# Performance work log

Hardware: AMD Instinct MI355X
Metric: run time of the kernel (lower is better)

## Reference

```python
import jax, jax.numpy as jnp
import numpy as np

N_LAYERS = 2
D_MODEL = 1024
D_INNER = 2 * D_MODEL
D_STATE = 16
D_CONV = 4
DT_RANK = D_MODEL // 16  # 64
B_SZ, L = 1, 2048
EPS = 1e-5


def layernorm(x, w, b):
    mu = jnp.mean(x, axis=-1, keepdims=True)
    var = jnp.mean(jnp.square(x - mu), axis=-1, keepdims=True)
    return (x - mu) * jax.lax.rsqrt(var + EPS) * w + b


def mamba(x, in_w, cw, cb, xp_w, dtp_w, dtp_b, A_log, Dp, out_w):
    # x: [B, L, D_MODEL]
    Bn, Ln, _ = x.shape
    xz = jnp.einsum('bld,ed->ble', x, in_w)          # [B,L,2*D_INNER]
    xc, z = jnp.split(xz, 2, axis=-1)
    # causal depthwise conv1d (kernel D_CONV)
    xp = jnp.pad(xc, ((0, 0), (D_CONV - 1, 0), (0, 0)))
    xc = sum(xp[:, k:k + Ln, :] * cw[:, k] for k in range(D_CONV)) + cb
    xc = jax.nn.silu(xc)
    dbl = jnp.einsum('ble,re->blr', xc, xp_w)        # [B,L,DT_RANK+2*D_STATE]
    dt, Bm, Cm = jnp.split(dbl, [DT_RANK, DT_RANK + D_STATE], axis=-1)
    dt = jax.nn.softplus(jnp.einsum('blr,er->ble', dt, dtp_w) + dtp_b)  # [B,L,E]
    A = -jnp.exp(A_log)                              # [E,N], strictly negative
    dA = jnp.exp(dt[..., None] * A)                  # [B,L,E,N]
    dBu = (dt * xc)[..., None] * Bm[:, :, None, :]   # [B,L,E,N]

    def step(h, inp):
        dA_t, dBu_t, C_t = inp
        h = dA_t * h + dBu_t                         # [B,E,N]
        y = jnp.einsum('ben,bn->be', h, C_t)
        return h, y

    h0 = jnp.zeros((Bn, D_INNER, D_STATE), dA.dtype)
    _, ys = jax.lax.scan(step, h0, (dA.transpose(1, 0, 2, 3),
                                    dBu.transpose(1, 0, 2, 3),
                                    Cm.transpose(1, 0, 2)))
    y = ys.transpose(1, 0, 2) + xc * Dp              # [B,L,E]
    y = y * jax.nn.silu(z)
    return jnp.einsum('ble,de->bld', y, out_w)       # [B,L,D_MODEL]


def setup_inputs() -> dict:
    key = jax.random.key(0)
    ks = jax.random.split(key, 12)
    s = 0.02
    dt_init = np.log(np.expm1(0.01)).astype(np.float32)  # softplus^-1(0.01)
    A_row = jnp.log(jnp.arange(1, D_STATE + 1, dtype=jnp.float32))
    return {
        'x': jax.random.normal(ks[0], (B_SZ, L, D_MODEL), jnp.float32),
        'ln_w': jnp.ones((N_LAYERS, D_MODEL), jnp.float32),
        'ln_b': jnp.zeros((N_LAYERS, D_MODEL), jnp.float32),
        'in_proj_w': jax.random.normal(ks[1], (N_LAYERS, 2 * D_INNER, D_MODEL)) * s,
        'conv_w': jax.random.normal(ks[2], (N_LAYERS, D_INNER, D_CONV)) * 0.2,
        'conv_b': jnp.zeros((N_LAYERS, D_INNER), jnp.float32),
        'x_proj_w': jax.random.normal(ks[3], (N_LAYERS, DT_RANK + 2 * D_STATE, D_INNER)) * s,
        'dt_proj_w': jax.random.normal(ks[4], (N_LAYERS, D_INNER, DT_RANK)) * (DT_RANK ** -0.5),
        'dt_proj_b': jnp.full((N_LAYERS, D_INNER), dt_init),
        'A_log': jnp.broadcast_to(A_row, (N_LAYERS, D_INNER, D_STATE)).copy(),
        'D_skip': jnp.ones((N_LAYERS, D_INNER), jnp.float32),
        'out_proj_w': jax.random.normal(ks[5], (N_LAYERS, D_MODEL, D_INNER)) * s,
        'norm_f_w': jnp.ones((D_MODEL,), jnp.float32),
        'norm_f_b': jnp.zeros((D_MODEL,), jnp.float32),
    }


def reference(x, ln_w, ln_b, in_proj_w, conv_w, conv_b, x_proj_w, dt_proj_w,
              dt_proj_b, A_log, D_skip, out_proj_w, norm_f_w, norm_f_b):
    for i in range(N_LAYERS):
        h = layernorm(x, ln_w[i], ln_b[i])
        h = mamba(h, in_proj_w[i], conv_w[i], conv_b[i], x_proj_w[i],
                  dt_proj_w[i], dt_proj_b[i], A_log[i], D_skip[i], out_proj_w[i])
        x = h + x  # residual (dropout/drop_path are identity in eval)
    return layernorm(x, norm_f_w, norm_f_b)
```

## Files before the change

kernel.cpp:

```cpp
#include <hip/hip_runtime.h>
#include <hip/hip_bf16.h>
#include <math.h>

#define LSEQ 2048
#define DMODEL 1024
#define DINNER 2048
#define DSTATE 16
#define DCONV 4
#define DTRANK 64
#define RPROJ 96

#define CHUNK 16
#define NCHUNK (LSEQ / CHUNK)

#define XSPLIT 4

typedef __attribute__((ext_vector_type(8))) short bf16x8;
typedef __attribute__((ext_vector_type(4))) float f32x4;

__device__ __forceinline__ float softplusf(float x) {
    return (x > 20.f) ? x : log1pf(__expf(x));
}
__device__ __forceinline__ float siluf(float x) {
    return x / (1.f + __expf(-x));
}
__device__ __forceinline__ short f2bf(float f) {
    union { float f; unsigned u; } v; v.f = f;
    unsigned r = v.u + 0x7FFFu + ((v.u >> 16) & 1u);
    return (short)(r >> 16);
}
__device__ __forceinline__ float bf2f(short h) {
    union { unsigned u; float f; } v;
    v.u = ((unsigned)(unsigned short)h) << 16;
    return v.f;
}

__device__ __forceinline__ void cvt8(const float* __restrict__ s,
                                     short* __restrict__ d, int i) {
    const float4 a = *(const float4*)(s + i);
    const float4 b = *(const float4*)(s + i + 4);
    alignas(16) short h[8];
    h[0] = f2bf(a.x); h[1] = f2bf(a.y); h[2] = f2bf(a.z); h[3] = f2bf(a.w);
    h[4] = f2bf(b.x); h[5] = f2bf(b.y); h[6] = f2bf(b.z); h[7] = f2bf(b.w);
    *(uint4*)(d + i) = *(const uint4*)h;
}

__global__ __launch_bounds__(256) void cvt_weights(
    const float* __restrict__ s0, short* __restrict__ d0, int n0,
    const float* __restrict__ s1, short* __restrict__ d1, int n1,
    const float* __restrict__ s2, short* __restrict__ d2, int n2,
    const float* __restrict__ s3, short* __restrict__ d3, int n3)
{
    int i = (blockIdx.x * 256 + threadIdx.x) * 8;
    if (i < n0) { cvt8(s0, d0, i); return; }
    i -= n0;
    if (i < n1) { cvt8(s1, d1, i); return; }
    i -= n1;
    if (i < n2) { cvt8(s2, d2, i); return; }
    i -= n2;
    if (i < n3) { cvt8(s3, d3, i); return; }
}

__global__ __launch_bounds__(256) void ln_kernel(
    const float* __restrict__ x, const float* __restrict__ w,
    const float* __restrict__ b, float* __restrict__ outf,
    short* __restrict__ outb)
{
    __shared__ float s1[256], s2[256];
    const int row = blockIdx.x;
    const int tid = threadIdx.x;
    const float* xr = x + (size_t)row * DMODEL;
    float v[4];
    float s = 0.f, sq = 0.f;
#pragma unroll
    for (int k = 0; k < 4; k++) {
        v[k] = xr[k * 256 + tid];
        s += v[k];
        sq += v[k] * v[k];
    }
    s1[tid] = s; s2[tid] = sq;
    __syncthreads();
    for (int off = 128; off > 0; off >>= 1) {
        if (tid < off) { s1[tid] += s1[tid + off]; s2[tid] += s2[tid + off]; }
        __syncthreads();
    }
    const float mu = s1[0] * (1.f / DMODEL);
    const float var = s2[0] * (1.f / DMODEL) - mu * mu;
    const float rstd = rsqrtf(var + 1e-5f);
#pragma unroll
    for (int k = 0; k < 4; k++) {
        const int i = k * 256 + tid;
        const float o = (v[k] - mu) * rstd * w[i] + b[i];
        if (outf) outf[(size_t)row * DMODEL + i] = o;
        if (outb) outb[(size_t)row * DMODEL + i] = f2bf(o);
    }
}

template<int MI, int NJ, int MODE>
__global__ __launch_bounds__(256) void gemm_mfma(
    const short* __restrict__ A, int lda,
    const short* __restrict__ W, int ldw,
    float* __restrict__ Cf, short* __restrict__ Cb, int ldc,
    int M, int N, int K,
    const float* __restrict__ resid)
{
    constexpr int BM = 32 * MI;
    constexpr int BN = 32 * NJ;
    constexpr int AISS = BM / 32;
    constexpr int WISS = BN / 32;
    __shared__ alignas(16) short As[BM * 64];
    __shared__ alignas(16) short Ws[BN * 64];

    const int tid = threadIdx.x;
    const int lane = tid & 63;
    const int w = tid >> 6;
    const int wr = w >> 1, wc = w & 1;
    const int row0 = blockIdx.y * BM;
    const int col0 = blockIdx.x * BN;
    const int kbeg = blockIdx.z * K;

    const int srow = tid >> 3;
    const int dch  = tid & 7;
    const int skch = (dch ^ (srow & 7)) * 8;

    f32x4 acc[MI][NJ];
#pragma unroll
    for (int i = 0; i < MI; i++)
#pragma unroll
        for (int j = 0; j < NJ; j++) acc[i][j] = (f32x4)0.f;

    const int lrow = lane & 15;
    const int q = lane >> 4;

    for (int kt = kbeg; kt < kbeg + K; kt += 64) {
        __syncthreads();
#pragma unroll
        for (int j = 0; j < AISS; j++) {
            const short* gp = A + (size_t)(row0 + j * 32 + srow) * lda + kt + skch;
            __builtin_amdgcn_global_load_lds(
                (const __attribute__((address_space(1))) void*)gp,
                (__attribute__((address_space(3))) void*)(&As[j * 2048 + tid * 8]),
                16, 0, 0);
        }
#pragma unroll
        for (int j = 0; j < WISS; j++) {
            const int wrow = col0 + j * 32 + srow;
            if (wrow < N) {
                const short* gp = W + (size_t)wrow * ldw + kt + skch;
                __builtin_amdgcn_global_load_lds(
                    (const __attribute__((address_space(1))) void*)gp,
                    (__attribute__((address_space(3))) void*)(&Ws[j * 2048 + tid * 8]),
                    16, 0, 0);
            }
        }
        __syncthreads();

#pragma unroll
        for (int ks = 0; ks < 2; ks++) {
            bf16x8 af[MI], bfr[NJ];
#pragma unroll
            for (int i = 0; i < MI; i++) {
                const int R = wr * (16 * MI) + i * 16 + lrow;
                const int pc = (ks * 4 + q) ^ (R & 7);
                af[i] = *(const bf16x8*)&As[R * 64 + pc * 8];
            }
#pragma unroll
            for (int j = 0; j < NJ; j++) {
                const int R = wc * (16 * NJ) + j * 16 + lrow;
                const int pc = (ks * 4 + q) ^ (R & 7);
                bfr[j] = *(const bf16x8*)&Ws[R * 64 + pc * 8];
            }
#pragma unroll
            for (int i = 0; i < MI; i++)
#pragma unroll
                for (int j = 0; j < NJ; j++)
                    acc[i][j] = __builtin_amdgcn_mfma_f32_16x16x32_bf16(
                        af[i], bfr[j], acc[i][j], 0, 0, 0);
        }
    }

    const int rbase = row0 + wr * (16 * MI);
    const int cbase = col0 + wc * (16 * NJ);
#pragma unroll
    for (int i = 0; i < MI; i++) {
#pragma unroll
        for (int j = 0; j < NJ; j++) {
            const int gcol = cbase + j * 16 + lrow;
            if (gcol < N) {
#pragma unroll
                for (int r = 0; r < 4; r++) {
                    const int grow = rbase + i * 16 + (lane >> 4) * 4 + r;
                    float v = acc[i][j][r];
                    if (MODE == 2) {
                        Cf[(size_t)grow * ldc + gcol] =
                            v + resid[(size_t)grow * ldc + gcol];
                    } else if (MODE == 3) {
                        Cb[(size_t)grow * ldc + gcol] = f2bf(v);
                    } else {
                        atomicAdd(&Cf[(size_t)grow * ldc + gcol], v);
                    }
                }
            }
        }
    }
}

__global__ __launch_bounds__(256) void dtproj_kernel(
    const float* __restrict__ dbl,
    const short* __restrict__ dtp_w,
    const float* __restrict__ dtp_b,
    short* __restrict__ dt_bf)
{
    __shared__ alignas(16) short As[64 * 32];
    __shared__ alignas(16) short Ws[128 * 32];
    const int tid = threadIdx.x;
    const int lane = tid & 63;
    const int w = tid >> 6;
    const int wr = w >> 1, wc = w & 1;
    const int row0 = blockIdx.y * 64;
    const int col0 = blockIdx.x * 128;
    const int srow = tid >> 2;
    const int skch = ((tid & 3) ^ ((srow >> 1) & 3)) * 8;
    const int lrow = lane & 15;
    const int q = lane >> 4;

    f32x4 acc[2][4];
#pragma unroll
    for (int i = 0; i < 2; i++)
#pragma unroll
        for (int j = 0; j < 4; j++) acc[i][j] = (f32x4)0.f;

#pragma unroll
    for (int kt = 0; kt < 64; kt += 32) {
        __syncthreads();
        {
            const float* gp = dbl + (size_t)(row0 + srow) * RPROJ + kt + skch;
            const float4 a = *(const float4*)gp;
            const float4 b = *(const float4*)(gp + 4);
            alignas(16) short h[8];
            h[0] = f2bf(a.x); h[1] = f2bf(a.y); h[2] = f2bf(a.z); h[3] = f2bf(a.w);
            h[4] = f2bf(b.x); h[5] = f2bf(b.y); h[6] = f2bf(b.z); h[7] = f2bf(b.w);
            *(uint4*)(As + tid * 8) = *(const uint4*)h;
        }
#pragma unroll
        for (int j = 0; j < 2; j++) {
            const short* gp = dtp_w + (size_t)(col0 + j * 64 + srow) * DTRANK + kt + skch;
            __builtin_amdgcn_global_load_lds(
                (const __attribute__((address_space(1))) void*)gp,
                (__attribute__((address_space(3))) void*)(&Ws[j * 2048 + tid * 8]),
                16, 0, 0);
        }
        __syncthreads();

        bf16x8 af[2], bfr[4];
#pragma unroll
        for (int i = 0; i < 2; i++) {
            const int R = wr * 32 + i * 16 + lrow;
            af[i] = *(const bf16x8*)&As[R * 32 + ((q ^ ((R >> 1) & 3)) * 8)];
        }
#pragma unroll
        for (int j = 0; j < 4; j++) {
            const int R = wc * 64 + j * 16 + lrow;
            bfr[j] = *(const bf16x8*)&Ws[R * 32 + ((q ^ ((R >> 1) & 3)) * 8)];
        }
#pragma unroll
        for (int i = 0; i < 2; i++)
#pragma unroll
            for (int j = 0; j < 4; j++)
                acc[i][j] = __builtin_amdgcn_mfma_f32_16x16x32_bf16(
                    af[i], bfr[j], acc[i][j], 0, 0, 0);
    }

    const int rbase = row0 + wr * 32;
    const int cbase = col0 + wc * 64;
#pragma unroll
    for (int i = 0; i < 2; i++)
#pragma unroll
        for (int j = 0; j < 4; j++) {
            const int gcol = cbase + j * 16 + lrow;
#pragma unroll
            for (int r = 0; r < 4; r++) {
                const int grow = rbase + i * 16 + (lane >> 4) * 4 + r;
                dt_bf[(size_t)grow * DINNER + gcol] =
                    f2bf(softplusf(acc[i][j][r] + dtp_b[gcol]));
            }
        }
}

__global__ __launch_bounds__(256) void conv_silu_kernel(
    const short* __restrict__ xzb, const float* __restrict__ cw,
    const float* __restrict__ cb, short* __restrict__ xcb,
    float* __restrict__ dbl_zero)
{
    const int g = blockIdx.x * 256 + threadIdx.x;
    if (g < (LSEQ * RPROJ) / 4)
        *(float4*)(dbl_zero + g * 4) = make_float4(0.f, 0.f, 0.f, 0.f);
    const int t = g >> 8;
    const int c0 = (g & 255) * 8;
    float acc[8];
#pragma unroll
    for (int j = 0; j < 8; j++) acc[j] = cb[c0 + j];
#pragma unroll
    for (int k = 0; k < DCONV; k++) {
        const int tt = t - (DCONV - 1) + k;
        if (tt >= 0) {
            const bf16x8 v = *(const bf16x8*)(xzb + (size_t)tt * (2 * DINNER) + c0);
#pragma unroll
            for (int j = 0; j < 8; j++)
                acc[j] += bf2f(v[j]) * cw[(c0 + j) * DCONV + k];
        }
    }
    alignas(16) short h[8];
#pragma unroll
    for (int j = 0; j < 8; j++) h[j] = f2bf(siluf(acc[j]));
    *(uint4*)(xcb + (size_t)t * DINNER + c0) = *(const uint4*)h;
}

__global__ __launch_bounds__(256) void scan_pass1(
    const short* __restrict__ dtb,
    const short* __restrict__ xcb,
    const float* __restrict__ dbl,
    const float* __restrict__ A_log,
    float* __restrict__ S,
    float* __restrict__ sumdt)
{
    const int e = blockIdx.x * 256 + threadIdx.x;
    const int c = blockIdx.y;
    float a[DSTATE];
#pragma unroll
    for (int n = 0; n < DSTATE; n++) a[n] = -__expf(A_log[(size_t)e * DSTATE + n]);
    float h[DSTATE];
#pragma unroll
    for (int n = 0; n < DSTATE; n++) h[n] = 0.f;
    float sd = 0.f;

    __shared__ float sBC[CHUNK][32];
    for (int i = threadIdx.x; i < CHUNK * 32; i += 256) {
        const int tl = i >> 5, j = i & 31;
        sBC[tl][j] = dbl[(size_t)(c * CHUNK + tl) * RPROJ + DTRANK + j];
    }
    __syncthreads();

    const size_t rb = (size_t)c * CHUNK * DINNER + e;
    short dt_c = dtb[rb], xc_c = xcb[rb];
#pragma unroll
    for (int tl = 0; tl < CHUNK; tl++) {
        short dt_n = 0, xc_n = 0;
        if (tl + 1 < CHUNK) {
            dt_n = dtb[rb + (size_t)(tl + 1) * DINNER];
            xc_n = xcb[rb + (size_t)(tl + 1) * DINNER];
        }
        const float dtv = bf2f(dt_c);
        const float du = dtv * bf2f(xc_c);
        sd += dtv;
#pragma unroll
        for (int n = 0; n < DSTATE; n++) {
            const float dA = __expf(dtv * a[n]);
            h[n] = dA * h[n] + du * sBC[tl][n];
        }
        dt_c = dt_n; xc_c = xc_n;
    }
    sumdt[(size_t)c * DINNER + e] = sd;
#pragma unroll
    for (int n = 0; n < DSTATE; n++)
        S[((size_t)c * DSTATE + n) * DINNER + e] = h[n];
}

__global__ __launch_bounds__(256) void scan_pass2(
    const float* __restrict__ A_log,
    const float* __restrict__ sumdt,
    float* __restrict__ S)
{
    const int idx = blockIdx.x * 256 + threadIdx.x;
    const int e = idx & (DINNER - 1);
    const int n = idx >> 11;
    const float a = -__expf(A_log[(size_t)e * DSTATE + n]);
    const size_t base = (size_t)n * DINNER + e;
    const size_t cstr = (size_t)DSTATE * DINNER;
    float H = 0.f;
    for (int c = 0; c < NCHUNK; c += 4) {
        const float sc0 = S[base + (size_t)(c + 0) * cstr];
        const float sc1 = S[base + (size_t)(c + 1) * cstr];
        const float sc2 = S[base + (size_t)(c + 2) * cstr];
        const float sc3 = S[base + (size_t)(c + 3) * cstr];
        const float sd0 = sumdt[(size_t)(c + 0) * DINNER + e];
        const float sd1 = sumdt[(size_t)(c + 1) * DINNER + e];
        const float sd2 = sumdt[(size_t)(c + 2) * DINNER + e];
        const float sd3 = sumdt[(size_t)(c + 3) * DINNER + e];
        S[base + (size_t)(c + 0) * cstr] = H;
        H = __expf(a * sd0) * H + sc0;
        S[base + (size_t)(c + 1) * cstr] = H;
        H = __expf(a * sd1) * H + sc1;
        S[base + (size_t)(c + 2) * cstr] = H;
        H = __expf(a * sd2) * H + sc2;
        S[base + (size_t)(c + 3) * cstr] = H;
        H = __expf(a * sd3) * H + sc3;
    }
}

__global__ __launch_bounds__(256) void scan_pass3(
    const short* __restrict__ dtb,
    const short* __restrict__ xcb,
    const float* __restrict__ dbl,
    const short* __restrict__ xzb,
    const float* __restrict__ A_log,
    const float* __restrict__ Dp,
    const float* __restrict__ S,
    short* __restrict__ yb)
{
    const int e = blockIdx.x * 256 + threadIdx.x;
    const int c = blockIdx.y;
    float a[DSTATE];
#pragma unroll
    for (int n = 0; n < DSTATE; n++) a[n] = -__expf(A_log[(size_t)e * DSTATE + n]);
    float h[DSTATE];
#pragma unroll
    for (int n = 0; n < DSTATE; n++)
        h[n] = S[((size_t)c * DSTATE + n) * DINNER + e];
    const float dskip = Dp[e];

    __shared__ float sBC[CHUNK][32];
    for (int i = threadIdx.x; i < CHUNK * 32; i += 256) {
        const int tl = i >> 5, j = i & 31;
        sBC[tl][j] = dbl[(size_t)(c * CHUNK + tl) * RPROJ + DTRANK + j];
    }
    __syncthreads();

    const size_t rb = (size_t)c * CHUNK * DINNER + e;
    const size_t zb = (size_t)c * CHUNK * (2 * DINNER) + DINNER + e;
    short dt_c = dtb[rb], xc_c = xcb[rb], z_c = xzb[zb];
#pragma unroll
    for (int tl = 0; tl < CHUNK; tl++) {
        short dt_n = 0, xc_n = 0, z_n = 0;
        if (tl + 1 < CHUNK) {
            dt_n = dtb[rb + (size_t)(tl + 1) * DINNER];
            xc_n = xcb[rb + (size_t)(tl + 1) * DINNER];
            z_n = xzb[zb + (size_t)(tl + 1) * (2 * DINNER)];
        }
        const float dtv = bf2f(dt_c);
        const float xcv = bf2f(xc_c);
        const float du = dtv * xcv;
        float yv = 0.f;
#pragma unroll
        for (int n = 0; n < DSTATE; n++) {
            const float dA = __expf(dtv * a[n]);
            h[n] = dA * h[n] + du * sBC[tl][n];
            yv += h[n] * sBC[tl][16 + n];
        }
        yv = (yv + xcv * dskip) * siluf(bf2f(z_c));
        yb[rb + (size_t)tl * DINNER] = f2bf(yv);
        dt_c = dt_n; xc_c = xc_n; z_c = z_n;
    }
}

extern "C" void kernel_launch(void* const* d_in, const int* in_sizes, int n_in,
                              void* d_out, int out_size, void* d_ws, size_t ws_size,
                              hipStream_t stream) {
    const float* x_in   = (const float*)d_in[0];
    const float* ln_w   = (const float*)d_in[1];
    const float* ln_b   = (const float*)d_in[2];
    const float* in_w   = (const float*)d_in[3];
    const float* conv_w = (const float*)d_in[4];
    const float* conv_b = (const float*)d_in[5];
    const float* xp_w   = (const float*)d_in[6];
    const float* dtp_w  = (const float*)d_in[7];
    const float* dtp_b  = (const float*)d_in[8];
    const float* A_log  = (const float*)d_in[9];
    const float* D_skip = (const float*)d_in[10];
    const float* out_w  = (const float*)d_in[11];
    const float* nf_w   = (const float*)d_in[12];
    const float* nf_b   = (const float*)d_in[13];
    float* out = (float*)d_out;

    float* w = (float*)d_ws;
    float* buf_x = w; w += (size_t)LSEQ * DMODEL;
    float* dbl   = w; w += (size_t)LSEQ * RPROJ;
    float* Sbuf  = w; w += (size_t)NCHUNK * DSTATE * DINNER;
    float* sumdt = w; w += (size_t)NCHUNK * DINNER;
    short* h_bf    = (short*)w; w += (size_t)LSEQ * DMODEL / 2;
    short* xz_bf   = (short*)w; w += (size_t)LSEQ * 2 * DINNER / 2;
    short* xc_bf   = (short*)w; w += (size_t)LSEQ * DINNER / 2;
    short* dt_bf   = (short*)w; w += (size_t)LSEQ * DINNER / 2;
    short* y_bf    = (short*)w; w += (size_t)LSEQ * DINNER / 2;
    short* in_w_bf  = (short*)w; w += (size_t)2 * (2 * DINNER) * DMODEL / 2;
    short* xp_w_bf  = (short*)w; w += (size_t)2 * RPROJ * DINNER / 2;
    short* dtp_w_bf = (short*)w; w += (size_t)2 * DINNER * DTRANK / 2;
    short* out_w_bf = (short*)w; w += (size_t)2 * DMODEL * DINNER / 2;

    {
        const int n1 = 2 * (2 * DINNER) * DMODEL;
        const int n2 = 2 * RPROJ * DINNER;
        const int n3 = 2 * DMODEL * DINNER;
        const int n4 = 2 * DINNER * DTRANK;
        const int total = n1 + n2 + n3 + n4;
        cvt_weights<<<dim3(total / (256 * 8)), dim3(256), 0, stream>>>(
            in_w, in_w_bf, n1, xp_w, xp_w_bf, n2,
            out_w, out_w_bf, n3, dtp_w, dtp_w_bf, n4);
    }

    for (int layer = 0; layer < 2; layer++) {
        const float* resid_src = (layer == 0) ? x_in : buf_x;
        ln_kernel<<<dim3(LSEQ), dim3(256), 0, stream>>>(
            resid_src, ln_w + layer * DMODEL, ln_b + layer * DMODEL,
            nullptr, h_bf);
        gemm_mfma<4, 4, 3><<<dim3((2 * DINNER) / 128, LSEQ / 128), dim3(256), 0, stream>>>(
            h_bf, DMODEL, in_w_bf + (size_t)layer * 2 * DINNER * DMODEL, DMODEL,
            nullptr, xz_bf, 2 * DINNER, LSEQ, 2 * DINNER, DMODEL, nullptr);
        conv_silu_kernel<<<dim3((LSEQ * DINNER / 8) / 256), dim3(256), 0, stream>>>(
            xz_bf, conv_w + (size_t)layer * DINNER * DCONV, conv_b + layer * DINNER,
            xc_bf, dbl);
        gemm_mfma<2, 2, 6><<<dim3(2, LSEQ / 64, XSPLIT), dim3(256), 0, stream>>>(
            xc_bf, DINNER, xp_w_bf + (size_t)layer * RPROJ * DINNER, DINNER,
            dbl, nullptr, RPROJ, LSEQ, RPROJ, DINNER / XSPLIT, nullptr);
        dtproj_kernel<<<dim3(DINNER / 128, LSEQ / 64), dim3(256), 0, stream>>>(
            dbl, dtp_w_bf + (size_t)layer * DINNER * DTRANK,
            dtp_b + layer * DINNER, dt_bf);
        const float* Al = A_log + (size_t)layer * DINNER * DSTATE;
        scan_pass1<<<dim3(DINNER / 256, NCHUNK), dim3(256), 0, stream>>>(
            dt_bf, xc_bf, dbl, Al, Sbuf, sumdt);
        scan_pass2<<<dim3((DINNER * DSTATE) / 256), dim3(256), 0, stream>>>(
            Al, sumdt, Sbuf);
        scan_pass3<<<dim3(DINNER / 256, NCHUNK), dim3(256), 0, stream>>>(
            dt_bf, xc_bf, dbl, xz_bf, Al, D_skip + layer * DINNER, Sbuf, y_bf);
        gemm_mfma<4, 2, 2><<<dim3(DMODEL / 64, LSEQ / 128), dim3(256), 0, stream>>>(
            y_bf, DINNER, out_w_bf + (size_t)layer * DMODEL * DINNER, DINNER,
            buf_x, nullptr, DMODEL, LSEQ, DMODEL, DINNER, resid_src);
    }
    ln_kernel<<<dim3(LSEQ), dim3(256), 0, stream>>>(buf_x, nf_w, nf_b, out, nullptr);
}
```

Baseline: 456.9 us.

## Fuse whole Mamba forward into one cooperative persistent kernel with grid syncs

Replaces the sequence of roughly twenty kernel launches with a single cooperative kernel of 512 blocks that runs every phase (weight conversion, layernorm, the GEMMs, conv, dt projection, the three scan passes) separated by grid.sync. LayerNorm now does one row per wavefront with shuffle reductions instead of a shared-memory tree. The out-projection GEMM tile shrinks to 64x64 and block-to-tile mappings are swizzled to fit the fixed grid. It aims to remove launch overhead and tail gaps between kernels, at the cost of grid-wide barriers, a fixed block count that may leave some phases underparallelised, and 2-blocks-per-CU occupancy limits. A fallback multi-kernel path is kept in case the cooperative launch is not possible.

After: 481.7 us. +5.4%, slower.

```diff
diff --git a/kernel.cpp b/kernel.cpp
--- a/kernel.cpp
+++ b/kernel.cpp
@@ -1,6 +1,9 @@
 #include <hip/hip_runtime.h>
+#include <hip/hip_cooperative_groups.h>
 #include <hip/hip_bf16.h>
 #include <math.h>
+
+namespace cg = cooperative_groups;
 
 #define LSEQ 2048
 #define DMODEL 1024
@@ -14,6 +17,7 @@
 #define NCHUNK (LSEQ / CHUNK)
 
 #define XSPLIT 4
+#define NBLK 512
 
 typedef __attribute__((ext_vector_type(8))) short bf16x8;
 typedef __attribute__((ext_vector_type(4))) float f32x4;
@@ -45,80 +49,82 @@
     *(uint4*)(d + i) = *(const uint4*)h;
 }
 
-__global__ __launch_bounds__(256) void cvt_weights(
-    const float* __restrict__ s0, short* __restrict__ d0, int n0,
-    const float* __restrict__ s1, short* __restrict__ d1, int n1,
-    const float* __restrict__ s2, short* __restrict__ d2, int n2,
-    const float* __restrict__ s3, short* __restrict__ d3, int n3)
-{
-    int i = (blockIdx.x * 256 + threadIdx.x) * 8;
-    if (i < n0) { cvt8(s0, d0, i); return; }
-    i -= n0;
-    if (i < n1) { cvt8(s1, d1, i); return; }
-    i -= n1;
-    if (i < n2) { cvt8(s2, d2, i); return; }
-    i -= n2;
-    if (i < n3) { cvt8(s3, d3, i); return; }
-}
-
-__global__ __launch_bounds__(256) void ln_kernel(
+__device__ __forceinline__ void cvt_phase(
+    const float* __restrict__ in_w, short* __restrict__ in_w_bf,
+    const float* __restrict__ xp_w, short* __restrict__ xp_w_bf,
+    const float* __restrict__ out_w, short* __restrict__ out_w_bf,
+    const float* __restrict__ dtp_w, short* __restrict__ dtp_w_bf,
+    int g0, int gstride)
+{
+    const int n1 = 2 * (2 * DINNER) * DMODEL;
+    const int n2 = 2 * RPROJ * DINNER;
+    const int n3 = 2 * DMODEL * DINNER;
+    const int n4 = 2 * DINNER * DTRANK;
+    const int total8 = (n1 + n2 + n3 + n4) / 8;
+    for (int g = g0; g < total8; g += gstride) {
+        int i = g * 8;
+        if (i < n1) { cvt8(in_w, in_w_bf, i); continue; }
+        i -= n1;
+        if (i < n2) { cvt8(xp_w, xp_w_bf, i); continue; }
+        i -= n2;
+        if (i < n3) { cvt8(out_w, out_w_bf, i); continue; }
+        i -= n3;
+        cvt8(dtp_w, dtp_w_bf, i);
+    }
+}
+
+__device__ __forceinline__ void ln_phase(
     const float* __restrict__ x, const float* __restrict__ w,
     const float* __restrict__ b, float* __restrict__ outf,
-    short* __restrict__ outb)
-{
-    __shared__ float s1[256], s2[256];
-    const int row = blockIdx.x;
-    const int tid = threadIdx.x;
+    short* __restrict__ outb, int bid, int tid)
+{
+    const int wv = tid >> 6, lane = tid & 63;
+    const int row = bid * 4 + wv;
     const float* xr = x + (size_t)row * DMODEL;
-    float v[4];
+    float v[16];
     float s = 0.f, sq = 0.f;
 #pragma unroll
-    for (int k = 0; k < 4; k++) {
-        v[k] = xr[k * 256 + tid];
+    for (int k = 0; k < 16; k++) {
+        v[k] = xr[k * 64 + lane];
         s += v[k];
         sq += v[k] * v[k];
     }
-    s1[tid] = s; s2[tid] = sq;
-    __syncthreads();
-    for (int off = 128; off > 0; off >>= 1) {
-        if (tid < off) { s1[tid] += s1[tid + off]; s2[tid] += s2[tid + off]; }
-        __syncthreads();
-    }
-    const float mu = s1[0] * (1.f / DMODEL);
-    const float var = s2[0] * (1.f / DMODEL) - mu * mu;
+#pragma unroll
+    for (int off = 32; off > 0; off >>= 1) {
+        s += __shfl_xor(s, off, 64);
+        sq += __shfl_xor(sq, off, 64);
+    }
+    const float mu = s * (1.f / DMODEL);
+    const float var = sq * (1.f / DMODEL) - mu * mu;
     const float rstd = rsqrtf(var + 1e-5f);
 #pragma unroll
-    for (int k = 0; k < 4; k++) {
-        const int i = k * 256 + tid;
+    for (int k = 0; k < 16; k++) {
+        const int i = k * 64 + lane;
         const float o = (v[k] - mu) * rstd * w[i] + b[i];
         if (outf) outf[(size_t)row * DMODEL + i] = o;
-        if (outb) outb[(size_t)row * DMODEL + i] = f2bf(o);
+        else      outb[(size_t)row * DMODEL + i] = f2bf(o);
     }
 }
 
 template<int MI, int NJ, int MODE>
-__global__ __launch_bounds__(256) void gemm_mfma(
+__device__ __forceinline__ void gemm_phase(
+    unsigned char* smemraw,
     const short* __restrict__ A, int lda,
     const short* __restrict__ W, int ldw,
     float* __restrict__ Cf, short* __restrict__ Cb, int ldc,
-    int M, int N, int K,
-    const float* __restrict__ resid)
+    int N, int K, int row0, int col0, int kbeg,
+    const float* __restrict__ resid, int tid)
 {
     constexpr int BM = 32 * MI;
     constexpr int BN = 32 * NJ;
     constexpr int AISS = BM / 32;
     constexpr int WISS = BN / 32;
-    __shared__ alignas(16) short As[BM * 64];
-    __shared__ alignas(16) short Ws[BN * 64];
-
-    const int tid = threadIdx.x;
+    short* As = (short*)smemraw;
+    short* Ws = (short*)(smemraw + (size_t)BM * 64 * 2);
+
     const int lane = tid & 63;
     const int w = tid >> 6;
     const int wr = w >> 1, wc = w & 1;
-    const int row0 = blockIdx.y * BM;
-    const int col0 = blockIdx.x * BN;
-    const int kbeg = blockIdx.z * K;
-
     const int srow = tid >> 3;
     const int dch  = tid & 7;
     const int skch = (dch ^ (srow & 7)) * 8;
@@ -205,20 +211,19 @@
     }
 }
 
-__global__ __launch_bounds__(256) void dtproj_kernel(
+__device__ __forceinline__ void dtproj_phase(
+    unsigned char* smemraw,
     const float* __restrict__ dbl,
     const short* __restrict__ dtp_w,
     const float* __restrict__ dtp_b,
-    short* __restrict__ dt_bf)
-{
-    __shared__ alignas(16) short As[64 * 32];
-    __shared__ alignas(16) short Ws[128 * 32];
-    const int tid = threadIdx.x;
+    short* __restrict__ dt_bf,
+    int row0, int col0, int tid)
+{
+    short* As = (short*)smemraw;
+    short* Ws = (short*)(smemraw + 64 * 32 * 2);
     const int lane = tid & 63;
     const int w = tid >> 6;
     const int wr = w >> 1, wc = w & 1;
-    const int row0 = blockIdx.y * 64;
-    const int col0 = blockIdx.x * 128;
     const int srow = tid >> 2;
     const int skch = ((tid & 3) ^ ((srow >> 1) & 3)) * 8;
     const int lrow = lane & 15;
@@ -287,45 +292,43 @@
         }
 }
 
-__global__ __launch_bounds__(256) void conv_silu_kernel(
+__device__ __forceinline__ void conv_phase(
     const short* __restrict__ xzb, const float* __restrict__ cw,
     const float* __restrict__ cb, short* __restrict__ xcb,
-    float* __restrict__ dbl_zero)
-{
-    const int g = blockIdx.x * 256 + threadIdx.x;
-    if (g < (LSEQ * RPROJ) / 4)
-        *(float4*)(dbl_zero + g * 4) = make_float4(0.f, 0.f, 0.f, 0.f);
-    const int t = g >> 8;
-    const int c0 = (g & 255) * 8;
-    float acc[8];
-#pragma unroll
-    for (int j = 0; j < 8; j++) acc[j] = cb[c0 + j];
-#pragma unroll
-    for (int k = 0; k < DCONV; k++) {
-        const int tt = t - (DCONV - 1) + k;
-        if (tt >= 0) {
-            const bf16x8 v = *(const bf16x8*)(xzb + (size_t)tt * (2 * DINNER) + c0);
-#pragma unroll
-            for (int j = 0; j < 8; j++)
-                acc[j] += bf2f(v[j]) * cw[(c0 + j) * DCONV + k];
-        }
-    }
-    alignas(16) short h[8];
-#pragma unroll
-    for (int j = 0; j < 8; j++) h[j] = f2bf(siluf(acc[j]));
-    *(uint4*)(xcb + (size_t)t * DINNER + c0) = *(const uint4*)h;
-}
-
-__global__ __launch_bounds__(256) void scan_pass1(
-    const short* __restrict__ dtb,
-    const short* __restrict__ xcb,
-    const float* __restrict__ dbl,
-    const float* __restrict__ A_log,
-    float* __restrict__ S,
-    float* __restrict__ sumdt)
-{
-    const int e = blockIdx.x * 256 + threadIdx.x;
-    const int c = blockIdx.y;
+    float* __restrict__ dbl_zero, int gid0, int gstride)
+{
+    for (int g = gid0; g < (LSEQ * DINNER) / 8; g += gstride) {
+        if (g < (LSEQ * RPROJ) / 4)
+            *(float4*)(dbl_zero + g * 4) = make_float4(0.f, 0.f, 0.f, 0.f);
+        const int t = g >> 8;
+        const int c0 = (g & 255) * 8;
+        float acc[8];
+#pragma unroll
+        for (int j = 0; j < 8; j++) acc[j] = cb[c0 + j];
+#pragma unroll
+        for (int k = 0; k < DCONV; k++) {
+            const int tt = t - (DCONV - 1) + k;
+            if (tt >= 0) {
+                const bf16x8 v = *(const bf16x8*)(xzb + (size_t)tt * (2 * DINNER) + c0);
+#pragma unroll
+                for (int j = 0; j < 8; j++)
+                    acc[j] += bf2f(v[j]) * cw[(c0 + j) * DCONV + k];
+            }
+        }
+        alignas(16) short h[8];
+#pragma unroll
+        for (int j = 0; j < 8; j++) h[j] = f2bf(siluf(acc[j]));
+        *(uint4*)(xcb + (size_t)t * DINNER + c0) = *(const uint4*)h;
+    }
+}
+
+__device__ __forceinline__ void scan1_job(
+    int eb, int c, int tid, float* sBC,
+    const short* __restrict__ dtb, const short* __restrict__ xcb,
+    const float* __restrict__ dbl, const float* __restrict__ A_log,
+    float* __restrict__ S, float* __restrict__ sumdt)
+{
+    const int e = eb * 256 + tid;
     float a[DSTATE];
 #pragma unroll
     for (int n = 0; n < DSTATE; n++) a[n] = -__expf(A_log[(size_t)e * DSTATE + n]);
@@ -334,10 +337,10 @@
     for (int n = 0; n < DSTATE; n++) h[n] = 0.f;
     float sd = 0.f;
 
-    __shared__ float sBC[CHUNK][32];
-    for (int i = threadIdx.x; i < CHUNK * 32; i += 256) {
+    __syncthreads();
+    for (int i = tid; i < CHUNK * 32; i += 256) {
         const int tl = i >> 5, j = i & 31;
-        sBC[tl][j] = dbl[(size_t)(c * CHUNK + tl) * RPROJ + DTRANK + j];
+        sBC[tl * 32 + j] = dbl[(size_t)(c * CHUNK + tl) * RPROJ + DTRANK + j];
     }
     __syncthreads();
 
@@ -356,7 +359,7 @@
 #pragma unroll
         for (int n = 0; n < DSTATE; n++) {
             const float dA = __expf(dtv * a[n]);
-            h[n] = dA * h[n] + du * sBC[tl][n];
+            h[n] = dA * h[n] + du * sBC[tl * 32 + n];
         }
         dt_c = dt_n; xc_c = xc_n;
     }
@@ -366,12 +369,10 @@
         S[((size_t)c * DSTATE + n) * DINNER + e] = h[n];
 }
 
-__global__ __launch_bounds__(256) void scan_pass2(
-    const float* __restrict__ A_log,
-    const float* __restrict__ sumdt,
-    float* __restrict__ S)
-{
-    const int idx = blockIdx.x * 256 + threadIdx.x;
+__device__ __forceinline__ void scan2_phase(
+    const float* __restrict__ A_log, const float* __restrict__ sumdt,
+    float* __restrict__ S, int idx)
+{
     const int e = idx & (DINNER - 1);
     const int n = idx >> 11;
     const float a = -__expf(A_log[(size_t)e * DSTATE + n]);
@@ -398,18 +399,14 @@
     }
 }
 
-__global__ __launch_bounds__(256) void scan_pass3(
-    const short* __restrict__ dtb,
-    const short* __restrict__ xcb,
-    const float* __restrict__ dbl,
-    const short* __restrict__ xzb,
-    const float* __restrict__ A_log,
-    const float* __restrict__ Dp,
-    const float* __restrict__ S,
-    short* __restrict__ yb)
-{
-    const int e = blockIdx.x * 256 + threadIdx.x;
-    const int c = blockIdx.y;
+__device__ __forceinline__ void scan3_job(
+    int eb, int c, int tid, float* sBC,
+    const short* __restrict__ dtb, const short* __restrict__ xcb,
+    const float* __restrict__ dbl, const short* __restrict__ xzb,
+    const float* __restrict__ A_log, const float* __restrict__ Dp,
+    const float* __restrict__ S, short* __restrict__ yb)
+{
+    const int e = eb * 256 + tid;
     float a[DSTATE];
 #pragma unroll
     for (int n = 0; n < DSTATE; n++) a[n] = -__expf(A_log[(size_t)e * DSTATE + n]);
@@ -419,10 +416,10 @@
         h[n] = S[((size_t)c * DSTATE + n) * DINNER + e];
     const float dskip = Dp[e];
 
-    __shared__ float sBC[CHUNK][32];
-    for (int i = threadIdx.x; i < CHUNK * 32; i += 256) {
+    __syncthreads();
+    for (int i = tid; i < CHUNK * 32; i += 256) {
         const int tl = i >> 5, j = i & 31;
-        sBC[tl][j] = dbl[(size_t)(c * CHUNK + tl) * RPROJ + DTRANK + j];
+        sBC[tl * 32 + j] = dbl[(size_t)(c * CHUNK + tl) * RPROJ + DTRANK + j];
     }
     __syncthreads();
 
@@ -444,8 +441,8 @@
 #pragma unroll
         for (int n = 0; n < DSTATE; n++) {
             const float dA = __expf(dtv * a[n]);
-            h[n] = dA * h[n] + du * sBC[tl][n];
-            yv += h[n] * sBC[tl][16 + n];
+            h[n] = dA * h[n] + du * sBC[tl * 32 + n];
+            yv += h[n] * sBC[tl * 32 + 16 + n];
         }
         yv = (yv + xcv * dskip) * siluf(bf2f(z_c));
         yb[rb + (size_t)tl * DINNER] = f2bf(yv);
@@ -453,25 +450,173 @@
     }
 }
 
+struct MegaParams {
+    const float *x_in, *ln_w, *ln_b, *in_w, *conv_w, *conv_b, *xp_w, *dtp_w,
+                *dtp_b, *A_log, *D_skip, *out_w, *nf_w, *nf_b;
+    float* out;
+    float *buf_x, *dbl, *Sbuf, *sumdt;
+    short *h_bf, *xz_bf, *xc_bf, *dt_bf, *y_bf;
+    short *in_w_bf, *xp_w_bf, *dtp_w_bf, *out_w_bf;
+};
+
+__global__ __launch_bounds__(256, 2) void mega_kernel(MegaParams p)
+{
+    cg::grid_group grid = cg::this_grid();
+    __shared__ alignas(16) unsigned char smem[32768];
+    const int bid = blockIdx.x;
+    const int tid = threadIdx.x;
+
+    cvt_phase(p.in_w, p.in_w_bf, p.xp_w, p.xp_w_bf, p.out_w, p.out_w_bf,
+              p.dtp_w, p.dtp_w_bf, bid * 256 + tid, NBLK * 256);
+    grid.sync();
+
+    for (int layer = 0; layer < 2; layer++) {
+        const float* resid = layer ? p.buf_x : p.x_in;
+        ln_phase(resid, p.ln_w + layer * DMODEL, p.ln_b + layer * DMODEL,
+                 nullptr, p.h_bf, bid, tid);
+        grid.sync();
+        {
+            const int swz = (bid & 7) * 64 + (bid >> 3);
+            const int tx = swz & 31, ty = swz >> 5;
+            gemm_phase<4, 4, 3>(smem,
+                p.h_bf, DMODEL,
+                p.in_w_bf + (size_t)layer * 2 * DINNER * DMODEL, DMODEL,
+                nullptr, p.xz_bf, 2 * DINNER,
+                2 * DINNER, DMODEL, ty * 128, tx * 128, 0, nullptr, tid);
+        }
+        grid.sync();
+        conv_phase(p.xz_bf, p.conv_w + (size_t)layer * DINNER * DCONV,
+                   p.conv_b + layer * DINNER, p.xc_bf, p.dbl,
+                   bid * 256 + tid, NBLK * 256);
+        grid.sync();
+        if (bid < 2 * 32 * XSPLIT) {
+            const int jx = bid & 1, jy = (bid >> 1) & 31, jz = bid >> 6;
+            gemm_phase<2, 2, 6>(smem,
+                p.xc_bf, DINNER,
+                p.xp_w_bf + (size_t)layer * RPROJ * DINNER, DINNER,
+                p.dbl, nullptr, RPROJ,
+                RPROJ, DINNER / XSPLIT, jy * 64, jx * 64,
+                jz * (DINNER / XSPLIT), nullptr, tid);
+        }
+        grid.sync();
+        {
+            const int jx = bid & 15, jy = bid >> 4;
+            dtproj_phase(smem, p.dbl,
+                         p.dtp_w_bf + (size_t)layer * DINNER * DTRANK,
+                         p.dtp_b + layer * DINNER, p.dt_bf,
+                         jy * 64, jx * 128, tid);
+        }
+        grid.sync();
+        {
+            const float* Al = p.A_log + (size_t)layer * DINNER * DSTATE;
+            float* sBC = (float*)smem;
+#pragma unroll
+            for (int jj = 0; jj < 2; jj++) {
+                const int job = bid * 2 + jj;
+                scan1_job(job & 7, job >> 3, tid, sBC,
+                          p.dt_bf, p.xc_bf, p.dbl, Al, p.Sbuf, p.sumdt);
+            }
+        }
+        grid.sync();
+        if (bid < (DINNER * DSTATE) / 256) {
+            const float* Al = p.A_log + (size_t)layer * DINNER * DSTATE;
+            scan2_phase(Al, p.sumdt, p.Sbuf, bid * 256 + tid);
+        }
+        grid.sync();
+        {
+            const float* Al = p.A_log + (size_t)layer * DINNER * DSTATE;
+            float* sBC = (float*)smem;
+#pragma unroll
+            for (int jj = 0; jj < 2; jj++) {
+                const int job = bid * 2 + jj;
+                scan3_job(job & 7, job >> 3, tid, sBC,
+                          p.dt_bf, p.xc_bf, p.dbl, p.xz_bf, Al,
+                          p.D_skip + layer * DINNER, p.Sbuf, p.y_bf);
+            }
+        }
+        grid.sync();
+        {
+            const int swz = (bid & 7) * 64 + (bid >> 3);
+            const int jx = swz & 15, jy = swz >> 4;
+            gemm_phase<2, 2, 2>(smem,
+                p.y_bf, DINNER,
+                p.out_w_bf + (size_t)layer * DMODEL * DINNER, DINNER,
+                p.buf_x, nullptr, DMODEL,
+                DMODEL, DINNER, jy * 64, jx * 64, 0, resid, tid);
+        }
+        grid.sync();
+    }
+    ln_phase(p.buf_x, p.nf_w, p.nf_b, p.out, nullptr, bid, tid);
+}
+
+__global__ __launch_bounds__(256) void cvt_g(
+    const float* in_w, short* in_w_bf, const float* xp_w, short* xp_w_bf,
+    const float* out_w, short* out_w_bf, const float* dtp_w, short* dtp_w_bf)
+{
+    cvt_phase(in_w, in_w_bf, xp_w, xp_w_bf, out_w, out_w_bf, dtp_w, dtp_w_bf,
+              blockIdx.x * 256 + threadIdx.x, gridDim.x * 256);
+}
+
+__global__ __launch_bounds__(256) void ln_g(
+    const float* x, const float* w, const float* b, float* outf, short* outb)
+{
+    ln_phase(x, w, b, outf, outb, blockIdx.x, threadIdx.x);
+}
+
+template<int MI, int NJ, int MODE>
+__global__ __launch_bounds__(256) void gemm_g(
+    const short* A, int lda, const short* W, int ldw,
+    float* Cf, short* Cb, int ldc, int N, int K, const float* resid)
+{
+    __shared__ alignas(16) unsigned char smem[(32 * MI + 32 * NJ) * 64 * 2];
+    gemm_phase<MI, NJ, MODE>(smem, A, lda, W, ldw, Cf, Cb, ldc, N, K,
+                             blockIdx.y * 32 * MI, blockIdx.x * 32 * NJ,
+                             blockIdx.z * K, resid, threadIdx.x);
+}
+
+__global__ __launch_bounds__(256) void conv_g(
+    const short* xzb, const float* cw, const float* cb, short* xcb,
+    float* dbl_zero)
+{
+    conv_phase(xzb, cw, cb, xcb, dbl_zero,
+               blockIdx.x * 256 + threadIdx.x, gridDim.x * 256);
+}
+
+__global__ __launch_bounds__(256) void dtproj_g(
+    const float* dbl, const short* dtp_w, const float* dtp_b, short* dt_bf)
+{
+    __shared__ alignas(16) unsigned char smem[(64 + 128) * 32 * 2];
+    dtproj_phase(smem, dbl, dtp_w, dtp_b, dt_bf,
+                 blockIdx.y * 64, blockIdx.x * 128, threadIdx.x);
+}
+
+__global__ __launch_bounds__(256) void scan1_g(
+    const short* dtb, const short* xcb, const float* dbl,
+    const float* A_log, float* S, float* sumdt)
+{
+    __shared__ float sBC[CHUNK * 32];
+    scan1_job(blockIdx.x, blockIdx.y, threadIdx.x, sBC,
+              dtb, xcb, dbl, A_log, S, sumdt);
+}
+
+__global__ __launch_bounds__(256) void scan2_g(
+    const float* A_log, const float* sumdt, float* S)
+{
+    scan2_phase(A_log, sumdt, S, blockIdx.x * 256 + threadIdx.x);
+}
+
+__global__ __launch_bounds__(256) void scan3_g(
+    const short* dtb, const short* xcb, const float* dbl, const short* xzb,
+    const float* A_log, const float* Dp, const float* S, short* yb)
+{
+    __shared__ float sBC[CHUNK * 32];
+    scan3_job(blockIdx.x, blockIdx.y, threadIdx.x, sBC,
+              dtb, xcb, dbl, xzb, A_log, Dp, S, yb);
+}
+
 extern "C" void kernel_launch(void* const* d_in, const int* in_sizes, int n_in,
                               void* d_out, int out_size, void* d_ws, size_t ws_size,
                               hipStream_t stream) {
-    const float* x_in   = (const float*)d_in[0];
-    const float* ln_w   = (const float*)d_in[1];
-    const float* ln_b   = (const float*)d_in[2];
-    const float* in_w   = (const float*)d_in[3];
-    const float* conv_w = (const float*)d_in[4];
-    const float* conv_b = (const float*)d_in[5];
-    const float* xp_w   = (const float*)d_in[6];
-    const float* dtp_w  = (const float*)d_in[7];
-    const float* dtp_b  = (const float*)d_in[8];
-    const float* A_log  = (const float*)d_in[9];
-    const float* D_skip = (const float*)d_in[10];
-    const float* out_w  = (const float*)d_in[11];
-    const float* nf_w   = (const float*)d_in[12];
-    const float* nf_b   = (const float*)d_in[13];
-    float* out = (float*)d_out;
-
     float* w = (float*)d_ws;
     float* buf_x = w; w += (size_t)LSEQ * DMODEL;
     float* dbl   = w; w += (size_t)LSEQ * RPROJ;
@@ -487,44 +632,82 @@
     short* dtp_w_bf = (short*)w; w += (size_t)2 * DINNER * DTRANK / 2;
     short* out_w_bf = (short*)w; w += (size_t)2 * DMODEL * DINNER / 2;
 
-    {
-        const int n1 = 2 * (2 * DINNER) * DMODEL;
-        const int n2 = 2 * RPROJ * DINNER;
-        const int n3 = 2 * DMODEL * DINNER;
-        const int n4 = 2 * DINNER * DTRANK;
-        const int total = n1 + n2 + n3 + n4;
-        cvt_weights<<<dim3(total / (256 * 8)), dim3(256), 0, stream>>>(
-            in_w, in_w_bf, n1, xp_w, xp_w_bf, n2,
-            out_w, out_w_bf, n3, dtp_w, dtp_w_bf, n4);
-    }
-
+    MegaParams p;
+    p.x_in   = (const float*)d_in[0];
+    p.ln_w   = (const float*)d_in[1];
+    p.ln_b   = (const float*)d_in[2];
+    p.in_w   = (const float*)d_in[3];
+    p.conv_w = (const float*)d_in[4];
+    p.conv_b = (const float*)d_in[5];
+    p.xp_w   = (const float*)d_in[6];
+    p.dtp_w  = (const float*)d_in[7];
+    p.dtp_b  = (const float*)d_in[8];
+    p.A_log  = (const float*)d_in[9];
+    p.D_skip = (const float*)d_in[10];
+    p.out_w  = (const float*)d_in[11];
+    p.nf_w   = (const float*)d_in[12];
+    p.nf_b   = (const float*)d_in[13];
+    p.out    = (float*)d_out;
+    p.buf_x = buf_x; p.dbl = dbl; p.Sbuf = Sbuf; p.sumdt = sumdt;
+    p.h_bf = h_bf; p.xz_bf = xz_bf; p.xc_bf = xc_bf; p.dt_bf = dt_bf;
+    p.y_bf = y_bf;
+    p.in_w_bf = in_w_bf; p.xp_w_bf = xp_w_bf; p.dtp_w_bf = dtp_w_bf;
+    p.out_w_bf = out_w_bf;
+
+    static int coop_state = -1;
+    if (coop_state == -1) {
+        int dev = 0;
+        (void)hipGetDevice(&dev);
+        hipDeviceProp_t prop;
+        int nb = 0;
+        if (hipGetDeviceProperties(&prop, dev) == hipSuccess &&
+            hipOccupancyMaxActiveBlocksPerMultiprocessor(
+                &nb, (const void*)mega_kernel, 256, 0) == hipSuccess &&
+            nb * prop.multiProcessorCount >= NBLK) {
+            coop_state = 1;
+        } else {
+            coop_state = 0;
+        }
+    }
+    if (coop_state == 1) {
+        void* args[] = { &p };
+        hipError_t e = hipLaunchCooperativeKernel(
+            (void*)mega_kernel, dim3(NBLK), dim3(256), args, 0, stream);
+        if (e == hipSuccess) return;
+        (void)hipGetLastError();
+        coop_state = 0;
+    }
+
+    cvt_g<<<dim3(6464), dim3(256), 0, stream>>>(
+        p.in_w, in_w_bf, p.xp_w, xp_w_bf, p.out_w, out_w_bf, p.dtp_w, dtp_w_bf);
     for (int layer = 0; layer < 2; layer++) {
-        const float* resid_src = (layer == 0) ? x_in : buf_x;
-        ln_kernel<<<dim3(LSEQ), dim3(256), 0, stream>>>(
-            resid_src, ln_w + layer * DMODEL, ln_b + layer * DMODEL,
+        const float* resid_src = (layer == 0) ? p.x_in : buf_x;
+        ln_g<<<dim3(NBLK), dim3(256), 0, stream>>>(
+            resid_src, p.ln_w + layer * DMODEL, p.ln_b + layer * DMODEL,
             nullptr, h_bf);
-        gemm_mfma<4, 4, 3><<<dim3((2 * DINNER) / 128, LSEQ / 128), dim3(256), 0, stream>>>(
+        gemm_g<4, 4, 3><<<dim3(32, 16), dim3(256), 0, stream>>>(
             h_bf, DMODEL, in_w_bf + (size_t)layer * 2 * DINNER * DMODEL, DMODEL,
-            nullptr, xz_bf, 2 * DINNER, LSEQ, 2 * DINNER, DMODEL, nullptr);
-        conv_silu_kernel<<<dim3((LSEQ * DINNER / 8) / 256), dim3(256), 0, stream>>>(
-            xz_bf, conv_w + (size_t)layer * DINNER * DCONV, conv_b + layer * DINNER,
-            xc_bf, dbl);
-        gemm_mfma<2, 2, 6><<<dim3(2, LSEQ / 64, XSPLIT), dim3(256), 0, stream>>>(
+            nullptr, xz_bf, 2 * DINNER, 2 * DINNER, DMODEL, nullptr);
+        conv_g<<<dim3(2048), dim3(256), 0, stream>>>(
+            xz_bf, p.conv_w + (size_t)layer * DINNER * DCONV,
+            p.conv_b + layer * DINNER, xc_bf, dbl);
+        gemm_g<2, 2, 6><<<dim3(2, 32, XSPLIT), dim3(256), 0, stream>>>(
             xc_bf, DINNER, xp_w_bf + (size_t)layer * RPROJ * DINNER, DINNER,
-            dbl, nullptr, RPROJ, LSEQ, RPROJ, DINNER / XSPLIT, nullptr);
-        dtproj_kernel<<<dim3(DINNER / 128, LSEQ / 64), dim3(256), 0, stream>>>(
+            dbl, nullptr, RPROJ, RPROJ, DINNER / XSPLIT, nullptr);
+        dtproj_g<<<dim3(16, 32), dim3(256), 0, stream>>>(
             dbl, dtp_w_bf + (size_t)layer * DINNER * DTRANK,
-            dtp_b + layer * DINNER, dt_bf);
-        const float* Al = A_log + (size_t)layer * DINNER * DSTATE;
-        scan_pass1<<<dim3(DINNER / 256, NCHUNK), dim3(256), 0, stream>>>(
+            p.dtp_b + layer * DINNER, dt_bf);
+        const float* Al = p.A_log + (size_t)layer * DINNER * DSTATE;
+        scan1_g<<<dim3(8, NCHUNK), dim3(256), 0, stream>>>(
             dt_bf, xc_bf, dbl, Al, Sbuf, sumdt);
-        scan_pass2<<<dim3((DINNER * DSTATE) / 256), dim3(256), 0, stream>>>(
+        scan2_g<<<dim3((DINNER * DSTATE) / 256), dim3(256), 0, stream>>>(
             Al, sumdt, Sbuf);
-        scan_pass3<<<dim3(DINNER / 256, NCHUNK), dim3(256), 0, stream>>>(
-            dt_bf, xc_bf, dbl, xz_bf, Al, D_skip + layer * DINNER, Sbuf, y_bf);
-        gemm_mfma<4, 2, 2><<<dim3(DMODEL / 64, LSEQ / 128), dim3(256), 0, stream>>>(
+        scan3_g<<<dim3(8, NCHUNK), dim3(256), 0, stream>>>(
+            dt_bf, xc_bf, dbl, xz_bf, Al, p.D_skip + layer * DINNER, Sbuf, y_bf);
+        gemm_g<2, 2, 2><<<dim3(16, 32), dim3(256), 0, stream>>>(
             y_bf, DINNER, out_w_bf + (size_t)layer * DMODEL * DINNER, DINNER,
-            buf_x, nullptr, DMODEL, LSEQ, DMODEL, DINNER, resid_src);
-    }
-    ln_kernel<<<dim3(LSEQ), dim3(256), 0, stream>>>(buf_x, nf_w, nf_b, out, nullptr);
-}
+            buf_x, nullptr, DMODEL, DMODEL, DINNER, resid_src);
+    }
+    ln_g<<<dim3(NBLK), dim3(256), 0, stream>>>(buf_x, p.nf_w, p.nf_b,
+                                               (float*)d_out, nullptr);
+}
```
